# Optimization experiments

Measured on AMD Instinct MI355X. Metric: run time of the kernel, lower is better.

Reference implementation:

```python
import jax, jax.numpy as jnp
import numpy as np

B, S, D, V, ND = 8, 512, 1024, 32000, 8


def setup_inputs() -> dict:
    key = jax.random.key(0)
    k1, k2, k3, k4 = jax.random.split(key, 4)
    scale = 0.02
    return {
        "hidden_states": jax.random.normal(k1, (B, S, D), dtype=jnp.float32),
        "domain_ids": jax.random.randint(k2, (B,), 0, ND + 1),  # index ND triggers default head
        "W_base": jax.random.normal(k3, (D, D), dtype=jnp.float32) * scale,
        "b_base": jnp.zeros((D,), dtype=jnp.float32),
        # slots 0..ND-1 are domain heads, slot ND is the default head
        "W_heads": jax.random.normal(k4, (ND + 1, D, V), dtype=jnp.float32) * scale,
        "b_heads": jnp.zeros((ND + 1, V), dtype=jnp.float32),
    }


def reference(hidden_states, domain_ids, W_base, b_base, W_heads, b_heads):
    # base_projection: Linear(D, D)
    hidden = jnp.einsum("bsd,de->bse", hidden_states, W_base) + b_base
    num_domains = W_heads.shape[0] - 1
    # out-of-range domain ids fall back to the default head (last slot)
    idx = jnp.where((domain_ids >= 0) & (domain_ids < num_domains), domain_ids, num_domains)
    Wg = W_heads[idx]              # [B, D, V] gathered per-example head weights
    bg = b_heads[idx]              # [B, V]
    out = jnp.einsum("bsd,bdv->bsv", hidden, Wg) + bg[:, None, :]
    return out
```

## Files before the change

kernel.cpp:

```cpp
#include <hip/hip_runtime.h>
#include <hip/hip_bf16.h>


#define BCNT 8
#define SLEN 512
#define DDIM 1024
#define VDIM 32000
#define NDOM 8

typedef __attribute__((ext_vector_type(4))) float f32x4;
typedef __attribute__((ext_vector_type(8))) short bf16x8;

static __device__ __forceinline__ unsigned short f2bf(float f) {
    union { float f; unsigned int u; } x; x.f = f;
    unsigned int u = x.u;
    return (unsigned short)((u + 0x7FFFu + ((u >> 16) & 1u)) >> 16);
}

static __device__ __forceinline__ unsigned int pack2(float lo, float hi) {
    float2 t; t.x = lo; t.y = hi;
    union { __hip_bfloat162 h; unsigned int u; } c;
    c.h = __float22bfloat162_rn(t);
    return c.u;
}

#define SBAR()   __builtin_amdgcn_s_barrier()
#define SCHED0() __builtin_amdgcn_sched_barrier(0)

__global__ __launch_bounds__(256)
void gemm1_k(const float* __restrict__ Af, const float* __restrict__ Bbase,
             const float* __restrict__ bias, __hip_bfloat16* __restrict__ Cb,
             int Mrows)
{
    __shared__ __align__(16) __hip_bfloat16 lds_a[128 * 64];
    __shared__ __align__(16) unsigned int   lds_b[32 * 128];

    const int tid  = threadIdx.x;
    const int lane = tid & 63;
    const int w    = tid >> 6;

    const int nwg = gridDim.x;
    const int bid = blockIdx.x;
    const int q   = nwg >> 3;
    const int sid = (bid & 7) * q + (bid >> 3);

    const int MT = Mrows >> 7;
    const int mt = sid % MT;
    const int nt = sid / MT;
    const int m0 = mt << 7;
    const int n0 = nt << 7;

    f32x4 acc[4][4];
    #pragma unroll
    for (int m = 0; m < 4; ++m)
        #pragma unroll
        for (int n = 0; n < 4; ++n)
            acc[m][n] = (f32x4)0.0f;

    const int wr = w >> 1, wc = w & 1;
    const int lr = lane & 15, lg = lane >> 4;

    for (int kt = 0; kt < DDIM / 64; ++kt) {
        const int kbase = kt * 64;

        #pragma unroll
        for (int t = 0; t < 8; ++t) {
            const int flat = (t * 256 + tid) * 4;
            const int row = flat >> 6, col = flat & 63;
            const float4 v = *(const float4*)(Af + (size_t)(m0 + row) * DDIM + kbase + col);
            uint2 pp;
            pp.x = pack2(v.x, v.y);
            pp.y = pack2(v.z, v.w);
            *(uint2*)(lds_a + flat) = pp;
        }

        #pragma unroll
        for (int t = 0; t < 4; ++t) {
            const int id = t * 256 + tid;
            const int kk = id >> 5;
            const int n  = (id & 31) << 2;
            const float* b0 = Bbase + (size_t)(kbase + 2 * kk) * DDIM + n0 + n;
            const float4 e = *(const float4*)b0;
            const float4 o = *(const float4*)(b0 + DDIM);
            uint4 pw;
            pw.x = pack2(e.x, o.x);
            pw.y = pack2(e.y, o.y);
            pw.z = pack2(e.z, o.z);
            pw.w = pack2(e.w, o.w);
            const int ns = n ^ ((kk & 4) << 2);
            *(uint4*)&lds_b[kk * 128 + ns] = pw;
        }

        __syncthreads();

        #pragma unroll
        for (int ks = 0; ks < 2; ++ks) {
            bf16x8 af[4], bfr[4];
            #pragma unroll
            for (int m = 0; m < 4; ++m) {
                const int row = wr * 64 + m * 16 + lr;
                const int k   = ks * 32 + lg * 8;
                af[m] = *(const bf16x8*)&lds_a[row * 64 + k];
            }
            #pragma unroll
            for (int n = 0; n < 4; ++n) {
                const int col = wc * 64 + n * 16 + lr;
                const int kkb = ks * 16 + lg * 4;
                union { unsigned int u[4]; bf16x8 v; } cvt;
                #pragma unroll
                for (int j = 0; j < 4; ++j) {
                    const int kk = kkb + j;
                    const int ns = col ^ ((kk & 4) << 2);
                    cvt.u[j] = lds_b[kk * 128 + ns];
                }
                bfr[n] = cvt.v;
            }
            #pragma unroll
            for (int m = 0; m < 4; ++m)
                #pragma unroll
                for (int n = 0; n < 4; ++n)
                    acc[m][n] = __builtin_amdgcn_mfma_f32_16x16x32_bf16(af[m], bfr[n], acc[m][n], 0, 0, 0);
        }

        __syncthreads();
    }

    #pragma unroll
    for (int m = 0; m < 4; ++m) {
        #pragma unroll
        for (int n = 0; n < 4; ++n) {
            const int col = n0 + wc * 64 + n * 16 + lr;
            const float bv = bias[col];
            #pragma unroll
            for (int r = 0; r < 4; ++r) {
                const int row = m0 + wr * 64 + m * 16 + lg * 4 + r;
                Cb[(size_t)row * DDIM + col] = __hip_bfloat16_raw{f2bf(acc[m][n][r] + bv)};
            }
        }
    }
}

__global__ __launch_bounds__(512, 2)
void gemm2_k(const __hip_bfloat16* __restrict__ A, const float* __restrict__ Wh,
             const float* __restrict__ bh, float* __restrict__ out,
             const int* __restrict__ dom)
{
    extern __shared__ __align__(16) char smem[];
    __hip_bfloat16* ldsA0 = (__hip_bfloat16*)smem;
    __hip_bfloat16* ldsA1 = (__hip_bfloat16*)(smem + 32768);
    unsigned int*   ldsB0 = (unsigned int*)(smem + 65536);
    unsigned int*   ldsB1 = (unsigned int*)(smem + 81920);

    const int tid  = threadIdx.x;
    const int lane = tid & 63;
    const int w    = tid >> 6;
    const int wr   = w >> 1;
    const int wc   = w & 1;
    const int lr   = lane & 15;
    const int lg   = lane >> 4;

    const int bid  = blockIdx.x;
    const int q    = gridDim.x >> 3;
    const int sid  = (bid & 7) * q + (bid >> 3);
    const int mt   = sid & 1;
    const int rest = sid >> 1;
    const int nt   = rest % 250;
    const int ex   = rest / 250;
    const int m0   = ex * SLEN + mt * 256;
    const int n0   = nt * 128;

    const int di  = dom[ex];
    const int hid = (di >= 0 && di < NDOM) ? di : NDOM;
    const float* Bp   = Wh + (size_t)hid * DDIM * (size_t)VDIM;
    const float* bias = bh + (size_t)hid * (size_t)VDIM;

    f32x4 acc[4][4];
    #pragma unroll
    for (int m = 0; m < 4; ++m)
        #pragma unroll
        for (int n = 0; n < 4; ++n)
            acc[m][n] = (f32x4)0.0f;

    const int nb  = (tid & 63) << 1;
    const int kb  = (tid >> 6) << 3;
    const int qb  = kb >> 1;
    const int bsw = (lane & 7) << 2;
    const int bslot = qb ^ bsw;

    float2 br[8];

    #define LOADB(KT) do {                                                         \
        const float* _p = Bp + (size_t)((KT) * 64 + kb) * VDIM + n0 + nb;          \
        _Pragma("unroll")                                                          \
        for (int j = 0; j < 8; ++j) br[j] = *(const float2*)(_p + (size_t)j * VDIM); \
    } while (0)

    #define WRITEB(LB) do {                                                        \
        uint4 w0, w1;                                                              \
        w0.x = pack2(br[0].x, br[1].x); w0.y = pack2(br[2].x, br[3].x);            \
        w0.z = pack2(br[4].x, br[5].x); w0.w = pack2(br[6].x, br[7].x);            \
        w1.x = pack2(br[0].y, br[1].y); w1.y = pack2(br[2].y, br[3].y);            \
        w1.z = pack2(br[4].y, br[5].y); w1.w = pack2(br[6].y, br[7].y);            \
        *(uint4*)&(LB)[nb * 32 + bslot]       = w0;                                \
        *(uint4*)&(LB)[(nb + 1) * 32 + bslot] = w1;                                \
    } while (0)

    #define STAGEA_H(LA, KT, H) do {                                               \
        _Pragma("unroll")                                                          \
        for (int i = 2*(H); i < 2*(H) + 2; ++i) {                                  \
            const int base_e = (i * 8 + w) * 512;                                  \
            const int flat   = base_e + lane * 8;                                  \
            const int row    = flat >> 6;                                          \
            const int kbyte  = (flat & 63) * 2;                                    \
            const int srck   = (kbyte ^ ((row & 7) << 4)) >> 1;                    \
            const __hip_bfloat16* src = A + (size_t)(m0 + row) * DDIM + (KT) * 64 + srck; \
            __builtin_amdgcn_global_load_lds(                                      \
                (const __attribute__((address_space(1))) unsigned int*)src,        \
                (__attribute__((address_space(3))) unsigned int*)((LA) + base_e),  \
                16, 0, 0);                                                         \
        }                                                                          \
    } while (0)

    #define READ_FRAGS(AF, BF, LA, LB, KS) do {                                    \
        _Pragma("unroll")                                                          \
        for (int m = 0; m < 4; ++m) {                                              \
            const int row = wr * 64 + m * 16 + lr;                                 \
            const int kby = (KS) * 64 + lg * 16;                                   \
            const int eff = kby ^ ((row & 7) << 4);                                \
            AF[m] = *(const bf16x8*)&(LA)[row * 64 + (eff >> 1)];                  \
        }                                                                          \
        _Pragma("unroll")                                                          \
        for (int n = 0; n < 4; ++n) {                                              \
            const int col  = wc * 64 + n * 16 + lr;                                \
            const int kkb  = (KS) * 16 + lg * 4;                                   \
            const int slot = kkb ^ (((col >> 1) & 7) << 2);                        \
            BF[n] = *(const bf16x8*)&(LB)[col * 32 + slot];                        \
        }                                                                          \
    } while (0)

    #define MFMA16(AF, BF) do {                                                    \
        _Pragma("unroll")                                                          \
        for (int m = 0; m < 4; ++m)                                                \
            _Pragma("unroll")                                                      \
            for (int n = 0; n < 4; ++n)                                            \
                acc[m][n] = __builtin_amdgcn_mfma_f32_16x16x32_bf16(AF[m], BF[n], acc[m][n], 0, 0, 0); \
    } while (0)

    LOADB(0);
    SCHED0();
    STAGEA_H(ldsA0, 0, 0);
    STAGEA_H(ldsA0, 0, 1);
    SCHED0();
    WRITEB(ldsB0);
    SCHED0();
    LOADB(1);
    SCHED0();
    asm volatile("s_waitcnt vmcnt(8) lgkmcnt(0)" ::: "memory");
    SCHED0();
    SBAR();

    for (int kt = 0; kt < 16; ++kt) {
        __hip_bfloat16* lA  = (kt & 1) ? ldsA1 : ldsA0;
        __hip_bfloat16* lAn = (kt & 1) ? ldsA0 : ldsA1;
        unsigned int*   lB  = (kt & 1) ? ldsB1 : ldsB0;
        unsigned int*   lBn = (kt & 1) ? ldsB0 : ldsB1;

        {
            bf16x8 af[4], bfr[4];
            READ_FRAGS(af, bfr, lA, lB, 0);
            SCHED0();
            if (kt < 15) { STAGEA_H(lAn, kt + 1, 0); SCHED0(); }
            SBAR();
            asm volatile("s_waitcnt lgkmcnt(0)" ::: "memory");
            SCHED0();
            __builtin_amdgcn_s_setprio(1);
            MFMA16(af, bfr);
            __builtin_amdgcn_s_setprio(0);
            SCHED0();
            SBAR();
        }

        {
            bf16x8 af[4], bfr[4];
            READ_FRAGS(af, bfr, lA, lB, 1);
            SCHED0();
            if (kt < 15) {
                STAGEA_H(lAn, kt + 1, 1);
                SCHED0();
                WRITEB(lBn);
                SCHED0();
            }
            if (kt < 14) { LOADB(kt + 2); SCHED0(); }
            SBAR();
            asm volatile("s_waitcnt lgkmcnt(0)" ::: "memory");
            SCHED0();
            __builtin_amdgcn_s_setprio(1);
            MFMA16(af, bfr);
            __builtin_amdgcn_s_setprio(0);
            SCHED0();
            if (kt < 14) {
                asm volatile("s_waitcnt vmcnt(8)" ::: "memory");
            } else if (kt == 14) {
                asm volatile("s_waitcnt vmcnt(0)" ::: "memory");
            }
            SCHED0();
            if (kt < 15) SBAR();
        }
    }

    #pragma unroll
    for (int n = 0; n < 4; ++n) {
        const int col = n0 + wc * 64 + n * 16 + lr;
        const float bv = bias[col];
        #pragma unroll
        for (int m = 0; m < 4; ++m) {
            #pragma unroll
            for (int r = 0; r < 4; ++r) {
                const int row = m0 + wr * 64 + m * 16 + lg * 4 + r;
                out[(size_t)row * VDIM + col] = acc[m][n][r] + bv;
            }
        }
    }

    #undef LOADB
    #undef WRITEB
    #undef STAGEA_H
    #undef READ_FRAGS
    #undef MFMA16
}

extern "C" void kernel_launch(void* const* d_in, const int* in_sizes, int n_in,
                              void* d_out, int out_size, void* d_ws, size_t ws_size,
                              hipStream_t stream)
{
    const float* hs  = (const float*)d_in[0];
    const int*   dom = (const int*)d_in[1];
    const float* Wb  = (const float*)d_in[2];
    const float* bb  = (const float*)d_in[3];
    const float* Wh  = (const float*)d_in[4];
    const float* bh  = (const float*)d_in[5];
    float* out = (float*)d_out;
    __hip_bfloat16* hidden = (__hip_bfloat16*)d_ws;

    const int M = BCNT * SLEN;

    const int g1 = (M / 128) * (DDIM / 128);
    hipLaunchKernelGGL(gemm1_k, dim3(g1), dim3(256), 0, stream, hs, Wb, bb, hidden, M);

    const int smem_bytes = 98304;
    static int attr_set = 0;
    if (!attr_set) {
        hipFuncSetAttribute((const void*)gemm2_k, hipFuncAttributeMaxDynamicSharedMemorySize, smem_bytes);
        attr_set = 1;
    }
    const int g2 = BCNT * (SLEN / 256) * (VDIM / 128);
    hipLaunchKernelGGL(gemm2_k, dim3(g2), dim3(512), smem_bytes, stream, hidden, Wh, bh, out, dom);
}
```

Measured before the change: 578.8 us.

## Split head GEMM k-tile into four quadrant phases and rotate B LDS swizzle

Restructures each 64-wide k-tile of the head GEMM from two k-half phases into four output-quadrant phases. Each phase reads 2x2 fragments covering both k-steps, runs 8 MFMAs, and interleaves A staging, B writes and B global loads across the phases. It also adds a column-dependent rotation to the B LDS slot swizzle to reduce bank conflicts. The aim is finer-grained overlap of memory traffic with MFMA work, at the cost of more barriers per tile and possibly more fragment register pressure.

```diff
diff --git a/kernel.cpp b/kernel.cpp
--- a/kernel.cpp
+++ b/kernel.cpp
@@ -185,7 +185,7 @@
     const int kb  = (tid >> 6) << 3;
     const int qb  = kb >> 1;
     const int bsw = (lane & 7) << 2;
-    const int bslot = qb ^ bsw;
+    const int bslot = ((qb ^ bsw) + (((nb >> 4) & 3) << 3)) & 31;
 
     float2 br[8];
 
@@ -221,29 +221,45 @@
         }                                                                          \
     } while (0)
 
-    #define READ_FRAGS(AF, BF, LA, LB, KS) do {                                    \
-        _Pragma("unroll")                                                          \
-        for (int m = 0; m < 4; ++m) {                                              \
-            const int row = wr * 64 + m * 16 + lr;                                 \
-            const int kby = (KS) * 64 + lg * 16;                                   \
-            const int eff = kby ^ ((row & 7) << 4);                                \
-            AF[m] = *(const bf16x8*)&(LA)[row * 64 + (eff >> 1)];                  \
+    #define PHASE(QM, QN, LA, LB) do {                                             \
+        bf16x8 af[2][2], bfr[2][2];                                                \
+        _Pragma("unroll")                                                          \
+        for (int m2 = 0; m2 < 2; ++m2) {                                           \
+            const int row = wr * 64 + ((QM)*2 + m2) * 16 + lr;                     \
+            _Pragma("unroll")                                                      \
+            for (int ks = 0; ks < 2; ++ks) {                                       \
+                const int eff = (ks * 64 + lg * 16) ^ ((row & 7) << 4);            \
+                af[m2][ks] = *(const bf16x8*)&(LA)[row * 64 + (eff >> 1)];         \
+            }                                                                      \
         }                                                                          \
         _Pragma("unroll")                                                          \
-        for (int n = 0; n < 4; ++n) {                                              \
-            const int col  = wc * 64 + n * 16 + lr;                                \
-            const int kkb  = (KS) * 16 + lg * 4;                                   \
-            const int slot = kkb ^ (((col >> 1) & 7) << 2);                        \
-            BF[n] = *(const bf16x8*)&(LB)[col * 32 + slot];                        \
+        for (int n2 = 0; n2 < 2; ++n2) {                                           \
+            const int col = wc * 64 + ((QN)*2 + n2) * 16 + lr;                     \
+            _Pragma("unroll")                                                      \
+            for (int ks = 0; ks < 2; ++ks) {                                       \
+                const int kkb  = ks * 16 + lg * 4;                                 \
+                const int slot = ((kkb ^ (((col >> 1) & 7) << 2))                  \
+                                  + (((col >> 4) & 3) << 3)) & 31;                 \
+                bfr[n2][ks] = *(const bf16x8*)&(LB)[col * 32 + slot];              \
+            }                                                                      \
         }                                                                          \
-    } while (0)
-
-    #define MFMA16(AF, BF) do {                                                    \
-        _Pragma("unroll")                                                          \
-        for (int m = 0; m < 4; ++m)                                                \
+        SCHED0();                                                                  \
+        SBAR();                                                                    \
+        asm volatile("s_waitcnt lgkmcnt(0)" ::: "memory");                         \
+        SCHED0();                                                                  \
+        __builtin_amdgcn_s_setprio(1);                                             \
+        _Pragma("unroll")                                                          \
+        for (int ks = 0; ks < 2; ++ks)                                             \
             _Pragma("unroll")                                                      \
-            for (int n = 0; n < 4; ++n)                                            \
-                acc[m][n] = __builtin_amdgcn_mfma_f32_16x16x32_bf16(AF[m], BF[n], acc[m][n], 0, 0, 0); \
+            for (int m2 = 0; m2 < 2; ++m2)                                         \
+                _Pragma("unroll")                                                  \
+                for (int n2 = 0; n2 < 2; ++n2)                                     \
+                    acc[(QM)*2 + m2][(QN)*2 + n2] =                                \
+                        __builtin_amdgcn_mfma_f32_16x16x32_bf16(                   \
+                            af[m2][ks], bfr[n2][ks],                               \
+                            acc[(QM)*2 + m2][(QN)*2 + n2], 0, 0, 0);               \
+        __builtin_amdgcn_s_setprio(0);                                             \
+        SCHED0();                                                                  \
     } while (0)
 
     LOADB(0);
@@ -265,46 +281,25 @@
         unsigned int*   lB  = (kt & 1) ? ldsB1 : ldsB0;
         unsigned int*   lBn = (kt & 1) ? ldsB0 : ldsB1;
 
-        {
-            bf16x8 af[4], bfr[4];
-            READ_FRAGS(af, bfr, lA, lB, 0);
-            SCHED0();
-            if (kt < 15) { STAGEA_H(lAn, kt + 1, 0); SCHED0(); }
-            SBAR();
-            asm volatile("s_waitcnt lgkmcnt(0)" ::: "memory");
-            SCHED0();
-            __builtin_amdgcn_s_setprio(1);
-            MFMA16(af, bfr);
-            __builtin_amdgcn_s_setprio(0);
+        if (kt < 15) { STAGEA_H(lAn, kt + 1, 0); SCHED0(); }
+        PHASE(0, 0, lA, lB);
+        SBAR();
+
+        if (kt < 15) { STAGEA_H(lAn, kt + 1, 1); SCHED0(); }
+        PHASE(0, 1, lA, lB);
+        SBAR();
+
+        if (kt < 15) { WRITEB(lBn); SCHED0(); }
+        PHASE(1, 0, lA, lB);
+        SBAR();
+
+        if (kt < 14) { LOADB(kt + 2); SCHED0(); }
+        PHASE(1, 1, lA, lB);
+        if (kt < 15) {
+            if (kt < 14) asm volatile("s_waitcnt vmcnt(8)" ::: "memory");
+            else         asm volatile("s_waitcnt vmcnt(0)" ::: "memory");
             SCHED0();
             SBAR();
-        }
-
-        {
-            bf16x8 af[4], bfr[4];
-            READ_FRAGS(af, bfr, lA, lB, 1);
-            SCHED0();
-            if (kt < 15) {
-                STAGEA_H(lAn, kt + 1, 1);
-                SCHED0();
-                WRITEB(lBn);
-                SCHED0();
-            }
-            if (kt < 14) { LOADB(kt + 2); SCHED0(); }
-            SBAR();
-            asm volatile("s_waitcnt lgkmcnt(0)" ::: "memory");
-            SCHED0();
-            __builtin_amdgcn_s_setprio(1);
-            MFMA16(af, bfr);
-            __builtin_amdgcn_s_setprio(0);
-            SCHED0();
-            if (kt < 14) {
-                asm volatile("s_waitcnt vmcnt(8)" ::: "memory");
-            } else if (kt == 14) {
-                asm volatile("s_waitcnt vmcnt(0)" ::: "memory");
-            }
-            SCHED0();
-            if (kt < 15) SBAR();
         }
     }
 
@@ -325,8 +320,7 @@
     #undef LOADB
     #undef WRITEB
     #undef STAGEA_H
-    #undef READ_FRAGS
-    #undef MFMA16
+    #undef PHASE
 }
 
 extern "C" void kernel_launch(void* const* d_in, const int* in_sizes, int n_in,
```

Result: slower. 638.4 us (+10.3%).
